# Performance work log

Measured on AMD Instinct MI355X. Metric: run time of the kernel, lower is better.

The kernel has to match this reference:

```python
import jax, jax.numpy as jnp
import numpy as np

B = 2
D = 256
NH = 8
DH = D // NH
L = 4
K = 2                       # sampling grid per box side
NP = K * K                  # sampled points per level
FF = 1024
NQ = 300
NE = 6
ND = 6
REF_SIZE = 4.0
SHAPES = ((64, 64), (32, 32), (16, 16), (8, 8))
S = sum(h * w for h, w in SHAPES)


def make_ref_windows():
    ws = []
    for (H, W) in SHAPES:
        y = (jnp.arange(1, H + 1, dtype=jnp.float32) - 0.5) / (H + 1e-6)
        x = (jnp.arange(1, W + 1, dtype=jnp.float32) - 0.5) / (W + 1e-6)
        yy, xx = jnp.meshgrid(y, x, indexing='ij')
        ctr = jnp.stack([xx, yy], -1).reshape(-1, 2)
        size = jnp.broadcast_to(jnp.array([REF_SIZE / W, REF_SIZE / H], jnp.float32), ctr.shape)
        ws.append(jnp.concatenate([ctr, size], -1))
    return jnp.broadcast_to(jnp.concatenate(ws, 0)[None], (B, S, 4))


def layernorm(x, g, b):
    m = jnp.mean(x, -1, keepdims=True)
    v = jnp.mean((x - m) ** 2, -1, keepdims=True)
    return (x - m) / jnp.sqrt(v + 1e-5) * g + b


def inverse_sigmoid(x, eps=1e-5):
    x = jnp.clip(x, eps, 1.0 - eps)
    return jnp.log(x / (1.0 - x))


def bilinear_sample(vl, pts, Hl, Wl):
    # vl: [B, Hl*Wl, NH, DH], pts: [B, N, NP, 2] normalized to [0,1]
    x = pts[..., 0] * Wl - 0.5
    y = pts[..., 1] * Hl - 0.5
    x0f = jnp.floor(x); y0f = jnp.floor(y)
    wx = x - x0f; wy = y - y0f
    x0 = x0f.astype(jnp.int32); y0 = y0f.astype(jnp.int32)
    Bn, N, P = x.shape

    def gather(yi, xi):
        valid = ((xi >= 0) & (xi < Wl) & (yi >= 0) & (yi < Hl)).astype(vl.dtype)
        idx = jnp.clip(yi, 0, Hl - 1) * Wl + jnp.clip(xi, 0, Wl - 1)
        g = jnp.take_along_axis(vl, idx.reshape(Bn, N * P, 1, 1), axis=1)
        return g.reshape(Bn, N, P, NH, DH) * valid[..., None, None]

    w00 = ((1 - wx) * (1 - wy))[..., None, None]
    w01 = (wx * (1 - wy))[..., None, None]
    w10 = ((1 - wx) * wy)[..., None, None]
    w11 = (wx * wy)[..., None, None]
    return (gather(y0, x0) * w00 + gather(y0, x0 + 1) * w01
            + gather(y0 + 1, x0) * w10 + gather(y0 + 1, x0 + 1) * w11)


def box_attention(q, memory, ref_windows, Wv, bv, Wa, ba, Wo, bo):
    # q: [B,N,D], memory: [B,S,D], ref_windows: [B,N,4] (cx,cy,w,h)
    Bn, N, _ = q.shape
    v = (memory @ Wv + bv).reshape(Bn, memory.shape[1], NH, DH)
    attn = jax.nn.softmax((q @ Wa + ba).reshape(Bn, N, NH, L * NP), axis=-1)
    g = (jnp.arange(K, dtype=jnp.float32) + 0.5) / K - 0.5   # grid fractions in box
    gy, gx = jnp.meshgrid(g, g, indexing='ij')
    grid = jnp.stack([gx.ravel(), gy.ravel()], -1)           # [NP,2]
    pts = ref_windows[:, :, None, :2] + grid[None, None] * ref_windows[:, :, None, 2:]
    out = jnp.zeros((Bn, N, NH, DH), q.dtype)
    start = 0
    for l, (Hl, Wl) in enumerate(SHAPES):
        sl = Hl * Wl
        sampled = bilinear_sample(v[:, start:start + sl], pts, Hl, Wl)  # [B,N,NP,NH,DH]
        out = out + jnp.einsum('bnphd,bnhp->bnhd', sampled, attn[..., l * NP:(l + 1) * NP])
        start += sl
    return out.reshape(Bn, N, D) @ Wo + bo


def mha(q_in, k_in, v_in, Wqkv, bqkv, Wo, bo):
    Bn, N, _ = q_in.shape
    q = (q_in @ Wqkv[:, :D] + bqkv[:D]).reshape(Bn, N, NH, DH)
    k = (k_in @ Wqkv[:, D:2 * D] + bqkv[D:2 * D]).reshape(Bn, N, NH, DH)
    v = (v_in @ Wqkv[:, 2 * D:] + bqkv[2 * D:]).reshape(Bn, N, NH, DH)
    a = jax.nn.softmax(jnp.einsum('bqhd,bkhd->bhqk', q, k) / jnp.sqrt(jnp.float32(DH)), axis=-1)
    o = jnp.einsum('bhqk,bkhd->bqhd', a, v).reshape(Bn, N, D)
    return o @ Wo + bo


def pos_embed_2d(coords):
    # coords: [B,N,2] -> [B,N,D] sine embedding (deformable-DETR style)
    npf = D // 2
    dim_t = 10000.0 ** (2.0 * (jnp.arange(npf) // 2) / npf)
    p = coords[..., None] * (2 * np.pi) / dim_t               # [B,N,2,npf]
    p = jnp.stack([jnp.sin(p[..., 0::2]), jnp.cos(p[..., 1::2])], -1)
    return p.reshape(coords.shape[0], coords.shape[1], 2 * npf)


def reference(src, pos, eWv, ebv, eWa, eba, eWo, ebo, eW1, eb1, eW2, eb2,
              en1g, en1b, en2g, en2b,
              dWqkv, dbqkv, dWso, dbso, dWv, dbv, dWa, dba, dWo, dbo,
              dW1, db1, dW2, db2, dn1g, dn1b, dn2g, dn2b, dn3g, dn3b,
              cls_w, cls_b, bb_w1, bb_b1, bb_w2, bb_b2, bb_w3, bb_b3,
              el_w, el_b, el_g, el_beta):
    ref_windows = make_ref_windows()
    out = src
    for i in range(NE):
        a = box_attention(out + pos, out, ref_windows, eWv[i], ebv[i], eWa[i], eba[i], eWo[i], ebo[i])
        out = layernorm(out + a, en1g[i], en1b[i])
        f = jax.nn.relu(out @ eW1[i] + eb1[i]) @ eW2[i] + eb2[i]
        out = layernorm(out + f, en2g[i], en2b[i])
    # proposal selection (topk + gather)
    valid = jnp.all((ref_windows[..., :2] > 0.01) & (ref_windows[..., :2] < 0.99), axis=-1)
    logits = (out @ cls_w + cls_b)[..., 0]
    logits = jnp.where(valid, logits, -65504.0)
    _, idx = jax.lax.top_k(logits, NQ)
    q_emb = jnp.take_along_axis(out, idx[..., None], axis=1)
    tgt = layernorm(jax.lax.stop_gradient(q_emb) @ el_w + el_b, el_g, el_beta)
    ref_sel = jnp.take_along_axis(ref_windows, idx[..., None], axis=1)
    h = jax.nn.relu(q_emb @ bb_w1 + bb_b1)
    h = jax.nn.relu(h @ bb_w2 + bb_b2)
    tmp = h @ bb_w3 + bb_b3 + inverse_sigmoid(ref_sel)
    out_ref = jax.lax.stop_gradient(jax.nn.sigmoid(tmp))
    query_pos = pos_embed_2d(out_ref[..., :2]) + pos_embed_2d(out_ref[..., 2:])
    # decoder
    x = tgt
    inter = []
    for i in range(ND):
        qk = x + query_pos
        sa = mha(qk, qk, x, dWqkv[i], dbqkv[i], dWso[i], dbso[i])
        x = layernorm(x + sa, dn1g[i], dn1b[i])
        ca = box_attention(x + query_pos, out, out_ref, dWv[i], dbv[i], dWa[i], dba[i], dWo[i], dbo[i])
        x = layernorm(x + ca, dn2g[i], dn2b[i])
        f = jax.nn.relu(x @ dW1[i] + db1[i]) @ dW2[i] + db2[i]
        x = layernorm(x + f, dn3g[i], dn3b[i])
        inter.append(x)
    return jnp.stack(inter)  # [ND, B, NQ, D]


def setup_inputs() -> dict:
    key = jax.random.key(0)
    kit = iter(jax.random.split(key, 80))
    def rn(shape, s=0.02):
        return jax.random.normal(next(kit), shape, jnp.float32) * s
    z = lambda *sh: jnp.zeros(sh, jnp.float32)
    o = lambda *sh: jnp.ones(sh, jnp.float32)
    A = NH * L * NP
    return dict(
        src=jax.random.normal(next(kit), (B, S, D), jnp.float32),
        pos=jax.random.normal(next(kit), (B, S, D), jnp.float32),
        eWv=rn((NE, D, D)), ebv=z(NE, D), eWa=rn((NE, D, A)), eba=z(NE, A),
        eWo=rn((NE, D, D)), ebo=z(NE, D),
        eW1=rn((NE, D, FF)), eb1=z(NE, FF), eW2=rn((NE, FF, D)), eb2=z(NE, D),
        en1g=o(NE, D), en1b=z(NE, D), en2g=o(NE, D), en2b=z(NE, D),
        dWqkv=rn((ND, D, 3 * D)), dbqkv=z(ND, 3 * D),
        dWso=rn((ND, D, D)), dbso=z(ND, D),
        dWv=rn((ND, D, D)), dbv=z(ND, D), dWa=rn((ND, D, A)), dba=z(ND, A),
        dWo=rn((ND, D, D)), dbo=z(ND, D),
        dW1=rn((ND, D, FF)), db1=z(ND, FF), dW2=rn((ND, FF, D)), db2=z(ND, D),
        dn1g=o(ND, D), dn1b=z(ND, D), dn2g=o(ND, D), dn2b=z(ND, D), dn3g=o(ND, D), dn3b=z(ND, D),
        cls_w=rn((D, 1)), cls_b=z(1),
        bb_w1=rn((D, D)), bb_b1=z(D), bb_w2=rn((D, D)), bb_b2=z(D),
        bb_w3=rn((D, 4)), bb_b3=z(4),
        el_w=rn((D, D)), el_b=z(D), el_g=o(D), el_beta=z(D),
    )
```

## Files before the change

kernel.cpp:

```cpp
#include <hip/hip_runtime.h>
#include <hip/hip_bf16.h>
#include <math.h>

typedef unsigned short u16;
typedef unsigned int u32;
typedef unsigned long long u64;

#define Bc   2
#define NHc  8
#define Sc   5440
#define NQc  300
#define NEc  6
#define NDc  6
#define FFc  1024
#define BSc  (Bc*Sc)
#define BNQc (Bc*NQc)

__device__ __forceinline__ float us2f(u16 u) {
    union { float f; unsigned v; } x; x.v = ((unsigned)u) << 16; return x.f;
}

__device__ __forceinline__ u16 f2bf(float f) {
    unsigned u = __float_as_uint(f);
    unsigned r = u + 0x7FFFu + ((u >> 16) & 1u);
    return (u16)(r >> 16);
}
__device__ __forceinline__ float bf2f(u16 u) { return us2f(u); }
__device__ __forceinline__ unsigned pk2(u16 a, u16 b) { return (unsigned)a | ((unsigned)b << 16); }

__device__ __forceinline__ size_t pidx(int row, int k) {
    return (size_t)(k >> 5) * ((size_t)BSc * 32) + ((size_t)row << 5) + (size_t)(k & 31);
}

__device__ __forceinline__ int xcd_swz(int orig, int nwg) {
    int xcd = orig & 7;
    int q = nwg >> 3, r = nwg & 7;
    int base = (xcd < r) ? xcd * (q + 1) : r * (q + 1) + (xcd - r) * q;
    return base + (orig >> 3);
}

using bf16x8 = __attribute__((ext_vector_type(8))) short;
using f32x4  = __attribute__((ext_vector_type(4))) float;

__global__ void k_detect(const u16* __restrict__ src, int* __restrict__ flag) {
    __shared__ int cnt;
    if (threadIdx.x == 0) cnt = 0;
    __syncthreads();
    u16 v = src[threadIdx.x];
    int e = (v >> 7) & 0xFF;
    int plaus = (e == 0) || (e >= 107 && e <= 131);
    atomicAdd(&cnt, plaus);
    __syncthreads();
    if (threadIdx.x == 0) *flag = (cnt >= 224) ? 1 : 0;
}

struct CvtArgs {
    const void* in[48];
    long off[48];
    int n[48];
    int cnt;
    long total;
    u64 skip;
};
__global__ void k_cvt_all8(CvtArgs args, float* __restrict__ out,
                           const int* __restrict__ flag) {
    long g = ((long)blockIdx.x * 256 + threadIdx.x) * 8;
    if (g >= args.total) return;
    int lo = 0, hi = args.cnt - 1;
    while (lo < hi) {
        int mid = (lo + hi + 1) >> 1;
        if (args.off[mid] <= g) lo = mid; else hi = mid - 1;
    }
    long local = g - args.off[lo];
    long n = (long)args.n[lo];
    float v[8];
#pragma unroll
    for (int j = 0; j < 8; ++j) v[j] = 0.f;
    if (*flag) {
        if ((args.skip >> lo) & 1) return;
        const u16* p = (const u16*)args.in[lo] + local;
        if (local + 8 <= n) {
            uint4 r = *(const uint4*)p;
            const u16* pu = (const u16*)&r;
#pragma unroll
            for (int j = 0; j < 8; ++j) v[j] = us2f(pu[j]);
        } else {
            for (int j = 0; j < 8; ++j)
                if (local + j < n) v[j] = us2f(p[j]);
        }
    } else {
        const float* p = (const float*)args.in[lo] + local;
        if (local + 8 <= n) {
            float4 a = ((const float4*)p)[0];
            float4 b = ((const float4*)p)[1];
            v[0] = a.x; v[1] = a.y; v[2] = a.z; v[3] = a.w;
            v[4] = b.x; v[5] = b.y; v[6] = b.z; v[7] = b.w;
        } else {
            for (int j = 0; j < 8; ++j)
                if (local + j < n) v[j] = p[j];
        }
    }
    float4 o0, o1;
    o0.x = v[0]; o0.y = v[1]; o0.z = v[2]; o0.w = v[3];
    o1.x = v[4]; o1.y = v[5]; o1.z = v[6]; o1.w = v[7];
    ((float4*)(out + g))[0] = o0;
    ((float4*)(out + g))[1] = o1;
}

__global__ void k_addf2(const float* __restrict__ a, const float* __restrict__ pos,
                        u16* __restrict__ ah, u16* __restrict__ al,
                        u16* __restrict__ ph, u16* __restrict__ pl, int n) {
    int i = blockIdx.x * 256 + threadIdx.x;
    if (i >= n) return;
    int row = i >> 8, k = i & 255;
    size_t px = pidx(row, k);
    float x = a[i];
    u16 h = f2bf(x);
    ah[px] = h;
    al[px] = f2bf(x - bf2f(h));
    float s = x + pos[i];
    u16 h2 = f2bf(s);
    ph[px] = h2;
    pl[px] = f2bf(s - bf2f(h2));
}

template<int RELU>
__global__ __launch_bounds__(256) void k_mgemm(
    const u16* __restrict__ Ah, const u16* __restrict__ Al,
    const float* __restrict__ W, const u16* __restrict__ Wraw, int ldw,
    size_t wstride,
    const float* __restrict__ bias, int bstride,
    float* __restrict__ C, size_t cstride,
    u16* __restrict__ Ch, u16* __restrict__ Cl,
    int ldc, int K,
    const int* __restrict__ flag) {
    __shared__ __align__(16) u16 lsAH[4096];
    __shared__ __align__(16) u16 lsAL[4096];
    __shared__ __align__(16) u16 lsBH[4096];
    __shared__ __align__(16) u16 lsBL[4096];
    const int t = threadIdx.x;
    int lin = blockIdx.x + gridDim.x * blockIdx.y;
    lin = xcd_swz(lin, gridDim.x * gridDim.y);
    const int row0 = (lin / gridDim.x) * 128, col0 = (lin % gridDim.x) * 128;
    const int z = blockIdx.z;
    const int fast = *flag;
    const size_t PSLAB = (size_t)BSc * 32;
    W += (size_t)z * wstride;
    Wraw += (size_t)z * wstride;
    C += (size_t)z * cstride;
    bias += (size_t)z * bstride;

    const int c0 = t, c1 = 256 + t;
    const size_t abase = (size_t)row0 * 32;
    const u16* a0h = Ah + abase + (size_t)c0 * 8;
    const u16* a1h = Ah + abase + (size_t)c1 * 8;
    const u16* a0l = Al + abase + (size_t)c0 * 8;
    const u16* a1l = Al + abase + (size_t)c1 * 8;
    const unsigned d0 = (((unsigned)c0 & ~3u) | (((unsigned)c0 & 3u) ^ (((unsigned)c0 >> 3) & 3u))) * 8u;
    const unsigned d1 = (((unsigned)c1 & ~3u) | (((unsigned)c1 & 3u) ^ (((unsigned)c1 >> 3) & 3u))) * 8u;

    const int bkp = t >> 4, bno = t & 15;
    const float* bp = W + (size_t)(bkp * 2) * ldw + col0 + bno * 8;
    const u16*  brp = Wraw + (size_t)(bkp * 2) * ldw + col0 + bno * 8;

    const int lane = t & 63;
    const int w = t >> 6;
    const int wr = (w >> 1) * 64, wc = (w & 1) * 64;
    const int kg = lane >> 4, lr = lane & 15;

    unsigned iaf[4];
#pragma unroll
    for (int mi = 0; mi < 4; ++mi) {
        int arow = wr + mi * 16 + lr;
        iaf[mi] = ((unsigned)(arow << 2) + ((unsigned)kg ^ (((unsigned)arow >> 1) & 3u))) * 8u;
    }

    f32x4 acc[4][4] = {};
    uint4 aU0h, aU1h, aU0l, aU1l;
    float4 bR[4];
    uint4 bU0, bU1;
    aU0h = *(const uint4*)a0h;
    aU1h = *(const uint4*)a1h;
    aU0l = *(const uint4*)a0l;
    aU1l = *(const uint4*)a1l;
    if (fast) {
        bU0 = *(const uint4*)brp;
        bU1 = *(const uint4*)(brp + ldw);
    } else {
        const float4* q0 = (const float4*)bp;
        const float4* q1 = (const float4*)(bp + ldw);
        bR[0] = q0[0]; bR[1] = q0[1]; bR[2] = q1[0]; bR[3] = q1[1];
    }

    for (int k0 = 0; k0 < K; k0 += 32) {
        if (k0) __syncthreads();
        *(uint4*)&lsAH[d0] = aU0h;
        *(uint4*)&lsAH[d1] = aU1h;
        *(uint4*)&lsAL[d0] = aU0l;
        *(uint4*)&lsAL[d1] = aU1l;
        {
            unsigned bb = (unsigned)(bkp >> 2) * 1024u + (unsigned)(bkp & 3) * 2u;
            if (fast) {
                const u16* e0 = (const u16*)&bU0;
                const u16* e1 = (const u16*)&bU1;
#pragma unroll
                for (int j = 0; j < 8; ++j) {
                    int slot = bno * 8 + (j ^ (bno & 7));
                    *(unsigned*)&lsBH[bb + (unsigned)slot * 8u] = pk2(e0[j], e1[j]);
                }
            } else {
                float e0f[8], e1f[8];
                *(float4*)&e0f[0] = bR[0]; *(float4*)&e0f[4] = bR[1];
                *(float4*)&e1f[0] = bR[2]; *(float4*)&e1f[4] = bR[3];
#pragma unroll
                for (int j = 0; j < 8; ++j) {
                    int slot = bno * 8 + (j ^ (bno & 7));
                    u16 h0 = f2bf(e0f[j]), h1 = f2bf(e1f[j]);
                    *(unsigned*)&lsBH[bb + (unsigned)slot * 8u] = pk2(h0, h1);
                    u16 l0 = f2bf(e0f[j] - bf2f(h0));
                    u16 l1 = f2bf(e1f[j] - bf2f(h1));
                    *(unsigned*)&lsBL[bb + (unsigned)slot * 8u] = pk2(l0, l1);
                }
            }
        }
        __syncthreads();
        if (k0 + 32 < K) {
            size_t soff = (size_t)((k0 >> 5) + 1) * PSLAB;
            aU0h = *(const uint4*)(a0h + soff);
            aU1h = *(const uint4*)(a1h + soff);
            aU0l = *(const uint4*)(a0l + soff);
            aU1l = *(const uint4*)(a1l + soff);
            if (fast) {
                bU0 = *(const uint4*)(brp + (size_t)(k0 + 32) * ldw);
                bU1 = *(const uint4*)(brp + (size_t)(k0 + 33) * ldw);
            } else {
                const float4* q0 = (const float4*)(bp + (size_t)(k0 + 32) * ldw);
                const float4* q1 = (const float4*)(bp + (size_t)(k0 + 33) * ldw);
                bR[0] = q0[0]; bR[1] = q0[1]; bR[2] = q1[0]; bR[3] = q1[1];
            }
        }
        bf16x8 aH[4], aL[4], bH[4], bL[4];
#pragma unroll
        for (int mi = 0; mi < 4; ++mi) {
            aH[mi] = *(const bf16x8*)&lsAH[iaf[mi]];
            aL[mi] = *(const bf16x8*)&lsAL[iaf[mi]];
        }
#pragma unroll
        for (int ni = 0; ni < 4; ++ni) {
            int c = wc + ni * 16 + lr;
            int slot = (c & ~7) | ((c ^ (c >> 3)) & 7);
            unsigned ib = (unsigned)kg * 1024u + (unsigned)slot * 8u;
            bH[ni] = *(const bf16x8*)&lsBH[ib];
            if (!fast) bL[ni] = *(const bf16x8*)&lsBL[ib];
        }
#pragma unroll
        for (int mi = 0; mi < 4; ++mi)
#pragma unroll
            for (int ni = 0; ni < 4; ++ni) {
                acc[mi][ni] = __builtin_amdgcn_mfma_f32_16x16x32_bf16(aH[mi], bH[ni], acc[mi][ni], 0, 0, 0);
                acc[mi][ni] = __builtin_amdgcn_mfma_f32_16x16x32_bf16(aL[mi], bH[ni], acc[mi][ni], 0, 0, 0);
            }
        if (!fast) {
#pragma unroll
            for (int mi = 0; mi < 4; ++mi)
#pragma unroll
                for (int ni = 0; ni < 4; ++ni)
                    acc[mi][ni] = __builtin_amdgcn_mfma_f32_16x16x32_bf16(aH[mi], bL[ni], acc[mi][ni], 0, 0, 0);
        }
    }
    const int rb = row0 + wr + (lane >> 4) * 4;
#pragma unroll
    for (int ni = 0; ni < 4; ++ni) {
        int cc = col0 + wc + ni * 16 + lr;
        float bv = bias[cc];
#pragma unroll
        for (int mi = 0; mi < 4; ++mi) {
#pragma unroll
            for (int r2 = 0; r2 < 4; ++r2) {
                int rr = rb + mi * 16 + r2;
                float v = acc[mi][ni][r2] + bv;
                if (RELU) v = fmaxf(v, 0.f);
                if (C) C[(size_t)rr * ldc + cc] = v;
                if (Ch) {
                    size_t px = pidx(rr, cc);
                    u16 h = f2bf(v);
                    Ch[px] = h;
                    Cl[px] = f2bf(v - bf2f(h));
                }
            }
        }
    }
}

template<int RELU>
__global__ __launch_bounds__(256) void k_dgemm(
    const float* __restrict__ A, int lda,
    const float* __restrict__ W, int ldw, int wcol0,
    const float* __restrict__ bias,
    float* __restrict__ C, int ldc,
    int M, int N, int K) {
    __shared__ float As[2][16][68];
    __shared__ float Bs[2][16][68];
    int t = threadIdx.x;
    int row0 = blockIdx.y * 64, col0 = blockIdx.x * 64;
    int ti = t >> 4, tj = t & 15;
    int arow = t >> 2, akq = (t & 3) << 2;
    int bk = t >> 4, bn = (t & 15) << 2;
    bool aok = (row0 + arow) < M;
    const float* ap = A + (size_t)(row0 + arow) * lda + akq;
    const float* bp = W + (size_t)bk * ldw + wcol0 + col0 + bn;
    float4 aR = aok ? *(const float4*)ap : make_float4(0.f, 0.f, 0.f, 0.f);
    float4 bR = *(const float4*)bp;
    As[0][akq + 0][arow] = aR.x;
    As[0][akq + 1][arow] = aR.y;
    As[0][akq + 2][arow] = aR.z;
    As[0][akq + 3][arow] = aR.w;
    *(float4*)&Bs[0][bk][bn] = bR;
    __syncthreads();
    int cur = 0;
    float acc[4][4] = {};
    for (int k0 = 0; k0 < K; k0 += 16) {
        bool more = (k0 + 16) < K;
        if (more) {
            aR = aok ? *(const float4*)(ap + k0 + 16) : make_float4(0.f, 0.f, 0.f, 0.f);
            bR = *(const float4*)(bp + (size_t)(k0 + 16) * ldw);
        }
#pragma unroll
        for (int k = 0; k < 16; ++k) {
            float a[4], b[4];
#pragma unroll
            for (int r = 0; r < 4; ++r) a[r] = As[cur][k][ti * 4 + r];
#pragma unroll
            for (int c = 0; c < 4; ++c) b[c] = Bs[cur][k][tj * 4 + c];
#pragma unroll
            for (int r = 0; r < 4; ++r)
#pragma unroll
                for (int c = 0; c < 4; ++c) acc[r][c] += a[r] * b[c];
        }
        if (more) {
            int nxt = cur ^ 1;
            As[nxt][akq + 0][arow] = aR.x;
            As[nxt][akq + 1][arow] = aR.y;
            As[nxt][akq + 2][arow] = aR.z;
            As[nxt][akq + 3][arow] = aR.w;
            *(float4*)&Bs[nxt][bk][bn] = bR;
            __syncthreads();
            cur = nxt;
        }
    }
    for (int r = 0; r < 4; ++r) {
        int rr = row0 + ti * 4 + r;
        if (rr >= M) continue;
        for (int c = 0; c < 4; ++c) {
            int cc = col0 + tj * 4 + c;
            float v = acc[r][c] + bias[cc];
            if (RELU) v = fmaxf(v, 0.f);
            C[(size_t)rr * ldc + cc] = v;
        }
    }
}

__global__ __launch_bounds__(256) void k_gemm4(
    const float* __restrict__ A, const float* __restrict__ W,
    const float* __restrict__ bias, const float* __restrict__ rsel,
    float* __restrict__ oref, int M, int K) {
    int row = blockIdx.x * 64 + (threadIdx.x >> 2);
    int col = threadIdx.x & 3;
    if (row >= M) return;
    float acc = 0.f;
    const float* a = A + (size_t)row * K;
    for (int k = 0; k < K; ++k) acc += a[k] * W[k * 4 + col];
    float tmp = acc + bias[col];
    float r = rsel[(size_t)row * 4 + col];
    r = fminf(fmaxf(r, 1e-5f), 1.f - 1e-5f);
    float v = tmp + logf(r / (1.f - r));
    oref[(size_t)row * 4 + col] = 1.f / (1.f + __expf(-v));
}

__global__ void k_ln(const float* __restrict__ a, const float* __restrict__ b,
                     const float* __restrict__ g, const float* __restrict__ be,
                     float* __restrict__ o,
                     u16* __restrict__ oh, u16* __restrict__ ol,
                     const float* __restrict__ padd, float* __restrict__ opadd,
                     u16* __restrict__ oph, u16* __restrict__ opl,
                     void* __restrict__ sdst, size_t soff,
                     const int* __restrict__ flag) {
    int row = blockIdx.x;
    int t = threadIdx.x;
    __shared__ float red[256];
    size_t ix = (size_t)row * 256 + t;
    float x = a[ix];
    if (b) x += b[ix];
    red[t] = x;
    __syncthreads();
    for (int s = 128; s > 0; s >>= 1) { if (t < s) red[t] += red[t + s]; __syncthreads(); }
    float mean = red[0] / 256.f;
    __syncthreads();
    float d = x - mean;
    red[t] = d * d;
    __syncthreads();
    for (int s = 128; s > 0; s >>= 1) { if (t < s) red[t] += red[t + s]; __syncthreads(); }
    float var = red[0] / 256.f;
    float y = d * rsqrtf(var + 1e-5f) * g[t] + be[t];
    o[ix] = y;
    if (oh) {
        size_t px = pidx(row, t);
        u16 h = f2bf(y);
        oh[px] = h;
        ol[px] = f2bf(y - bf2f(h));
    }
    if (padd) {
        float z = y + padd[ix];
        if (opadd) opadd[ix] = z;
        if (oph) {
            size_t px = pidx(row, t);
            u16 h = f2bf(z);
            oph[px] = h;
            opl[px] = f2bf(z - bf2f(h));
        }
    }
    if (sdst) {
        if (*flag) ((__hip_bfloat16*)sdst)[soff + ix] = __float2bfloat16(y);
        else       ((float*)sdst)[soff + ix] = y;
    }
}

__global__ void k_refw(float* __restrict__ rw) {
    int s = blockIdx.x * 256 + threadIdx.x;
    if (s >= Sc) return;
    int start, HW;
    if (s < 4096)      { start = 0;    HW = 64; }
    else if (s < 5120) { start = 4096; HW = 32; }
    else if (s < 5376) { start = 5120; HW = 16; }
    else               { start = 5376; HW = 8;  }
    int loc = s - start;
    int i = loc / HW, j = loc % HW;
    rw[s * 4 + 0] = (j + 0.5f) / ((float)HW + 1e-6f);
    rw[s * 4 + 1] = (i + 0.5f) / ((float)HW + 1e-6f);
    rw[s * 4 + 2] = 4.0f / (float)HW;
    rw[s * 4 + 3] = 4.0f / (float)HW;
}

__global__ __launch_bounds__(256) void k_box_sample4(
    const float* __restrict__ v, const float* __restrict__ attn,
    const float* __restrict__ refw, int ref_bs,
    float* __restrict__ out, u16* __restrict__ outh, u16* __restrict__ outl,
    int N) {
    const int t = threadIdx.x;
    const int qi = t >> 6, lane = t & 63;
    const int blk = xcd_swz(blockIdx.x, gridDim.x);
    const int n = blk * 4 + qi;
    const int b = blockIdx.y;
    if (n >= N) return;
    const float* arow = attn + ((size_t)b * N + n) * 128;
    float2 wl = *(const float2*)(arow + lane * 2);
    float m = fmaxf(wl.x, wl.y);
#pragma unroll
    for (int d2 = 1; d2 < 8; d2 <<= 1) m = fmaxf(m, __shfl_xor(m, d2, 8));
    float e0 = __expf(wl.x - m), e1 = __expf(wl.y - m);
    float s = e0 + e1;
#pragma unroll
    for (int d2 = 1; d2 < 8; d2 <<= 1) s += __shfl_xor(s, d2, 8);
    float inv = 1.f / s;
    e0 *= inv; e1 *= inv;

    const float* rw = refw + (size_t)ref_bs * b + (size_t)n * 4;
    float cx = rw[0], cy = rw[1], bw = rw[2], bh = rw[3];
    const float* vb = v + (size_t)b * Sc * 256 + lane * 4;
    float4 acc = make_float4(0.f, 0.f, 0.f, 0.f);
    int start = 0;
    const int HWs[4] = {64, 32, 16, 8};
#pragma unroll
    for (int l = 0; l < 4; ++l) {
        int HW = HWs[l];
#pragma unroll
        for (int p = 0; p < 4; ++p) {
            float gx = (p & 1) ? 0.25f : -0.25f;
            float gy = (p >> 1) ? 0.25f : -0.25f;
            float x = (cx + gx * bw) * (float)HW - 0.5f;
            float y = (cy + gy * bh) * (float)HW - 0.5f;
            float x0f = floorf(x), y0f = floorf(y);
            float wx = x - x0f, wy = y - y0f;
            int x0 = (int)x0f, y0 = (int)y0f;
            float4 smp = make_float4(0.f, 0.f, 0.f, 0.f);
            if (x0 >= 0 && x0 < HW && y0 >= 0 && y0 < HW) {
                float4 g4 = *(const float4*)(vb + (size_t)(start + y0 * HW + x0) * 256);
                float wgt = (1.f - wx) * (1.f - wy);
                smp.x += wgt * g4.x; smp.y += wgt * g4.y; smp.z += wgt * g4.z; smp.w += wgt * g4.w;
            }
            if (x0 + 1 >= 0 && x0 + 1 < HW && y0 >= 0 && y0 < HW) {
                float4 g4 = *(const float4*)(vb + (size_t)(start + y0 * HW + x0 + 1) * 256);
                float wgt = wx * (1.f - wy);
                smp.x += wgt * g4.x; smp.y += wgt * g4.y; smp.z += wgt * g4.z; smp.w += wgt * g4.w;
            }
            if (x0 >= 0 && x0 < HW && y0 + 1 >= 0 && y0 + 1 < HW) {
                float4 g4 = *(const float4*)(vb + (size_t)(start + (y0 + 1) * HW + x0) * 256);
                float wgt = (1.f - wx) * wy;
                smp.x += wgt * g4.x; smp.y += wgt * g4.y; smp.z += wgt * g4.z; smp.w += wgt * g4.w;
            }
            if (x0 + 1 >= 0 && x0 + 1 < HW && y0 + 1 >= 0 && y0 + 1 < HW) {
                float4 g4 = *(const float4*)(vb + (size_t)(start + (y0 + 1) * HW + x0 + 1) * 256);
                float wgt = wx * wy;
                smp.x += wgt * g4.x; smp.y += wgt * g4.y; smp.z += wgt * g4.z; smp.w += wgt * g4.w;
            }
            const int idx = l * 4 + p;
            float wsel = (idx & 1) ? e1 : e0;
            float wv = __shfl(wsel, (lane & ~7) | (idx >> 1), 64);
            acc.x += wv * smp.x; acc.y += wv * smp.y;
            acc.z += wv * smp.z; acc.w += wv * smp.w;
        }
        start += HW * HW;
    }
    if (out) {
        size_t obase = ((size_t)b * N + n) * 256 + lane * 4;
        *(float4*)(out + obase) = acc;
    }
    if (outh) {
        size_t px = pidx(b * N + n, lane * 4);
        ushort4 h, lo;
        h.x = f2bf(acc.x); h.y = f2bf(acc.y); h.z = f2bf(acc.z); h.w = f2bf(acc.w);
        lo.x = f2bf(acc.x - bf2f(h.x)); lo.y = f2bf(acc.y - bf2f(h.y));
        lo.z = f2bf(acc.z - bf2f(h.z)); lo.w = f2bf(acc.w - bf2f(h.w));
        *(ushort4*)(outh + px) = h;
        *(ushort4*)(outl + px) = lo;
    }
}

__global__ void k_cls(const float* __restrict__ x, const float* __restrict__ w,
                      const float* __restrict__ cb, const float* __restrict__ rw,
                      float* __restrict__ logits) {
    int row = blockIdx.x;
    int t = threadIdx.x;
    __shared__ float red[256];
    red[t] = x[(size_t)row * 256 + t] * w[t];
    __syncthreads();
    for (int s = 128; s > 0; s >>= 1) { if (t < s) red[t] += red[t + s]; __syncthreads(); }
    if (t == 0) {
        int s = row % Sc;
        float cx = rw[s * 4], cy = rw[s * 4 + 1];
        bool valid = (cx > 0.01f) && (cx < 0.99f) && (cy > 0.01f) && (cy < 0.99f);
        logits[row] = valid ? (red[0] + cb[0]) : -65504.0f;
    }
}

__global__ void k_topk(const float* __restrict__ logits, int* __restrict__ idxout) {
    int b = blockIdx.x;
    int t = threadIdx.x;
    __shared__ unsigned keys[Sc];
    __shared__ int hist[256];
    __shared__ int suf[257];
    __shared__ unsigned sprefix;
    __shared__ int sR;
    __shared__ int cnt;
    __shared__ u64 cand[512];
    for (int i = t; i < Sc; i += 256) {
        union { float f; unsigned u; } x;
        x.f = logits[(size_t)b * Sc + i];
        unsigned u = x.u;
        keys[i] = (u & 0x80000000u) ? ~u : (u | 0x80000000u);
    }
    if (t == 0) { sprefix = 0; sR = NQc; suf[256] = 0; }
    __syncthreads();
    for (int shift = 24; shift >= 0; shift -= 8) {
        hist[t] = 0;
        __syncthreads();
        unsigned pref = sprefix;
        int R = sR;
        unsigned pmask = (shift == 24) ? 0u : (0xFFFFFFFFu << (shift + 8));
        for (int i = t; i < Sc; i += 256) {
            unsigned kk = keys[i];
            if ((kk & pmask) == (pref & pmask))
                atomicAdd(&hist[(kk >> shift) & 255], 1);
        }
        __syncthreads();
        suf[t] = hist[t];
        __syncthreads();
        for (int s2 = 1; s2 < 256; s2 <<= 1) {
            int vv = suf[t] + ((t + s2 < 256) ? suf[t + s2] : 0);
            __syncthreads();
            suf[t] = vv;
            __syncthreads();
        }
        if (suf[t] >= R && suf[t + 1] < R) {
            sR = R - suf[t + 1];
            sprefix = pref | ((unsigned)t << shift);
        }
        __syncthreads();
    }
    unsigned T = sprefix;
    if (t == 0) cnt = 0;
    __syncthreads();
    for (int i = t; i < Sc; i += 256) {
        unsigned kk = keys[i];
        if (kk >= T) {
            int slot = atomicAdd(&cnt, 1);
            if (slot < 512)
                cand[slot] = ~((((u64)kk) << 32) | (u64)(0xFFFFFFFFu - (unsigned)i));
        }
    }
    __syncthreads();
    int total = cnt < 512 ? cnt : 512;
    for (int i = t; i < 512; i += 256)
        if (i >= total) cand[i] = 0xFFFFFFFFFFFFFFFFull;
    __syncthreads();
    for (int i = t; i < 512; i += 256) {
        if (i >= total) continue;
        u64 mine = cand[i];
        int rank = 0;
        for (int j = 0; j < 512; ++j) rank += (cand[j] < mine) ? 1 : 0;
        if (rank < NQc) {
            u64 c = ~mine;
            idxout[b * NQc + rank] = (int)(0xFFFFFFFFu - (unsigned)(c & 0xFFFFFFFFull));
        }
    }
}

__global__ void k_gather(const float* __restrict__ x, const float* __restrict__ rw,
                         const int* __restrict__ idx, float* __restrict__ qemb,
                         float* __restrict__ refsel) {
    int q = blockIdx.x, b = blockIdx.y;
    int t = threadIdx.x;
    int id = idx[b * NQc + q];
    qemb[((size_t)b * NQc + q) * 256 + t] = x[((size_t)b * Sc + id) * 256 + t];
    if (t < 4) refsel[((size_t)b * NQc + q) * 4 + t] = rw[id * 4 + t];
}

__global__ void k_qpos(const float* __restrict__ outref, float* __restrict__ qpos) {
    int n = blockIdx.x, b = blockIdx.y;
    int t = threadIdx.x;
    const float* orf = outref + ((size_t)b * NQc + n) * 4;
    int c = t >> 7;
    int j = (t & 127) >> 1;
    int si = t & 1;
    float tj = powf(10000.f, (float)j / 64.f);
    float sc = 6.283185307179586f / tj;
    float v1 = orf[c] * sc;
    float v2 = orf[2 + c] * sc;
    float r = si ? (cosf(v1) + cosf(v2)) : (sinf(v1) + sinf(v2));
    qpos[((size_t)b * NQc + n) * 256 + t] = r;
}

#define NSPL 10
#define SPLW 30
__global__ __launch_bounds__(256) void k_mha2(
    const float* __restrict__ qk, const float* __restrict__ v,
    float* __restrict__ opart, float* __restrict__ mlpart) {
    __shared__ float lsK[SPLW][256];
    __shared__ float lsV[SPLW][256];
    const int t = threadIdx.x;
    const int h = t >> 5, ql = t & 31;
    const int b = blockIdx.y, z = blockIdx.z;
    const int n = blockIdx.x * 32 + ql;
    const bool qok = n < NQc;
    const int kstart = z * SPLW;
    for (int f = t; f < SPLW * 64; f += 256) {
        int r = f >> 6, c4 = f & 63;
        int krow = kstart + r;
        float4 kv = *(const float4*)(qk + (size_t)(b * NQc + krow) * 512 + 256 + c4 * 4);
        float4 vv = *(const float4*)(v + (size_t)(b * NQc + krow) * 256 + c4 * 4);
        *(float4*)&lsK[r][c4 * 4] = kv;
        *(float4*)&lsV[r][c4 * 4] = vv;
    }
    __syncthreads();
    float q[32];
    {
        const float* qp = qk + (size_t)(b * NQc + (qok ? n : 0)) * 512 + h * 32;
#pragma unroll
        for (int j4 = 0; j4 < 8; ++j4) {
            float4 f = ((const float4*)qp)[j4];
            q[j4 * 4 + 0] = f.x; q[j4 * 4 + 1] = f.y;
            q[j4 * 4 + 2] = f.z; q[j4 * 4 + 3] = f.w;
        }
    }
    const float scale = 0.17677669529663688f;
    float s[SPLW];
#pragma unroll
    for (int kk = 0; kk < SPLW; ++kk) {
        float acc = 0.f;
        const float* kr = &lsK[kk][h * 32];
#pragma unroll
        for (int j4 = 0; j4 < 8; ++j4) {
            float4 kf = ((const float4*)kr)[j4];
            acc += q[j4*4+0]*kf.x + q[j4*4+1]*kf.y + q[j4*4+2]*kf.z + q[j4*4+3]*kf.w;
        }
        s[kk] = acc * scale;
    }
    float m = s[0];
#pragma unroll
    for (int kk = 1; kk < SPLW; ++kk) m = fmaxf(m, s[kk]);
    float o[32];
#pragma unroll
    for (int j = 0; j < 32; ++j) o[j] = 0.f;
    float l = 0.f;
#pragma unroll
    for (int kk = 0; kk < SPLW; ++kk) {
        float e = __expf(s[kk] - m);
        l += e;
        const float* vr = &lsV[kk][h * 32];
#pragma unroll
        for (int j4 = 0; j4 < 8; ++j4) {
            float4 vf = ((const float4*)vr)[j4];
            o[j4*4+0] += e * vf.x; o[j4*4+1] += e * vf.y;
            o[j4*4+2] += e * vf.z; o[j4*4+3] += e * vf.w;
        }
    }
    if (qok) {
        float* op = opart + ((size_t)z * BNQc + (size_t)b * NQc + n) * 256 + h * 32;
#pragma unroll
        for (int j4 = 0; j4 < 8; ++j4) {
            float4 f;
            f.x = o[j4*4+0]; f.y = o[j4*4+1]; f.z = o[j4*4+2]; f.w = o[j4*4+3];
            ((float4*)op)[j4] = f;
        }
        float* mlp = mlpart + ((size_t)z * BNQc + (size_t)b * NQc + n) * 16 + h * 2;
        mlp[0] = m; mlp[1] = l;
    }
}

__global__ void k_mha_comb(const float* __restrict__ opart, const float* __restrict__ mlpart,
                           float* __restrict__ out) {
    int row = blockIdx.x;
    int t = threadIdx.x;
    int h = t >> 5;
    float mm[NSPL], ll[NSPL];
    float M = -3.0e38f;
#pragma unroll
    for (int z = 0; z < NSPL; ++z) {
        mm[z] = mlpart[((size_t)z * BNQc + row) * 16 + h * 2];
        ll[z] = mlpart[((size_t)z * BNQc + row) * 16 + h * 2 + 1];
        M = fmaxf(M, mm[z]);
    }
    float denom = 0.f, osum = 0.f;
#pragma unroll
    for (int z = 0; z < NSPL; ++z) {
        float a = __expf(mm[z] - M);
        denom += ll[z] * a;
        osum += opart[((size_t)z * BNQc + row) * 256 + t] * a;
    }
    out[(size_t)row * 256 + t] = osum / denom;
}

extern "C" void kernel_launch(void* const* d_in, const int* in_sizes, int n_in,
                              void* d_out, int out_size, void* d_ws, size_t ws_size,
                              hipStream_t stream) {
    char* base = (char*)d_ws;
    size_t off = 0;
    auto allocB = [&](size_t bytes) {
        char* p = base + off;
        off = (off + bytes + 255) & ~(size_t)255;
        return p;
    };
    int* flag = (int*)allocB(16);
    auto allocF = [&](size_t n) { return (float*)allocB(n * 4); };
    auto allocH = [&](size_t n) { return (u16*)allocB(n * 2); };

    k_detect<<<1, 256, 0, stream>>>((const u16*)d_in[0], flag);

    CvtArgs ca;
    long acc = 0;
    int ninp = n_in < 48 ? n_in : 48;
    for (int i = 0; i < 48; ++i) {
        int idx2 = i < ninp ? i : ninp - 1;
        ca.in[i] = d_in[idx2];
        ca.n[i] = (i < ninp) ? in_sizes[i] : 0;
        ca.off[i] = acc;
        acc += ((long)ca.n[i] + 63) & ~63L;
    }
    ca.cnt = 48;
    ca.total = acc;
    ca.skip = (1ull << 2) | (1ull << 4) | (1ull << 6) | (1ull << 8) |
              (1ull << 10) | (1ull << 20);
    float* cvtbase = allocF((size_t)acc);
    k_cvt_all8<<<(int)((acc / 8 + 255) / 256), 256, 0, stream>>>(ca, cvtbase, flag);
    float* F[48];
    for (int i = 0; i < 48; ++i) F[i] = cvtbase + ca.off[i];

    const size_t BSD = (size_t)BSc * 256;
    float* enc    = F[0];
    u16* encH  = allocH(BSD);  u16* encL  = allocH(BSD);
    u16* pbufH = allocH(BSD);  u16* pbufL = allocH(BSD);
    u16* tbufH = allocH(BSD);  u16* tbufL = allocH(BSD);
    u16* ffnhH = allocH((size_t)BSc * FFc);
    u16* ffnhL = allocH((size_t)BSc * FFc);
    float* vbuf   = allocF(BSD);
    float* vbuf6  = allocF((size_t)NDc * BSD);
    float* gout   = allocF(BSD);
    float* attnb  = allocF((size_t)BSc * 128);
    float* refw   = allocF(Sc * 4);
    float* logit  = allocF(BSc);
    int*   idx    = (int*)allocB(BNQc * 4);
    float* qemb   = allocF((size_t)BNQc * 256);
    float* rsel   = allocF(BNQc * 4);
    float* xbuf   = allocF((size_t)BNQc * 256);
    float* qposb  = allocF((size_t)BNQc * 256);
    float* dqk    = allocF((size_t)BNQc * 256);
    float* dqk512 = allocF((size_t)BNQc * 512);
    float* dv     = allocF((size_t)BNQc * 256);
    float* dt1    = allocF((size_t)BNQc * 256);
    float* dt2    = allocF((size_t)BNQc * 256);
    float* datt   = allocF((size_t)BNQc * 128);
    float* dffnh  = allocF((size_t)BNQc * FFc);
    float* h1f    = allocF((size_t)BNQc * 256);
    float* h2f    = allocF((size_t)BNQc * 256);
    float* oref   = allocF(BNQc * 4);
    float* opart  = allocF((size_t)NSPL * BNQc * 256);
    float* mlpart = allocF((size_t)NSPL * BNQc * 16);
    (void)ws_size; (void)out_size;

    auto MG = [&](int relu, const u16* Ah, const u16* Al, int widx, size_t woff, int ldw,
                  const float* bias, float* Cf, u16* Ch, u16* Cl, int ldc, int N, int K,
                  int nz, size_t wstride, int bstride, size_t cstride) {
        const float* Wf = F[widx] + woff;
        const u16* Wraw = (const u16*)d_in[widx] + woff;
        dim3 g(N / 128, BSc / 128, nz);
        if (relu) k_mgemm<1><<<g, 256, 0, stream>>>(Ah, Al, Wf, Wraw, ldw, wstride,
                                                    bias, bstride, Cf, cstride, Ch, Cl, ldc, K, flag);
        else      k_mgemm<0><<<g, 256, 0, stream>>>(Ah, Al, Wf, Wraw, ldw, wstride,
                                                    bias, bstride, Cf, cstride, Ch, Cl, ldc, K, flag);
    };
    auto DG = [&](int relu, const float* A, int lda, const float* W, int ldw, int wcol0,
                  const float* bias, float* C, int ldc, int M, int N, int K) {
        dim3 g(N / 64, (M + 63) / 64);
        if (relu) k_dgemm<1><<<g, 256, 0, stream>>>(A, lda, W, ldw, wcol0, bias, C, ldc, M, N, K);
        else      k_dgemm<0><<<g, 256, 0, stream>>>(A, lda, W, ldw, wcol0, bias, C, ldc, M, N, K);
    };

    const int nBSD = (int)BSD;
    k_refw<<<(Sc + 255) / 256, 256, 0, stream>>>(refw);
    k_addf2<<<(nBSD + 255) / 256, 256, 0, stream>>>(enc, F[1], encH, encL, pbufH, pbufL, nBSD);

    for (int i = 0; i < NEc; ++i) {
        MG(0, encH, encL, 2, (size_t)i * 65536, 256, F[3] + i * 256, vbuf, nullptr, nullptr,
           256, 256, 256, 1, 0, 0, 0);
        MG(0, pbufH, pbufL, 4, (size_t)i * 32768, 128, F[5] + i * 128, attnb, nullptr, nullptr,
           128, 128, 256, 1, 0, 0, 0);
        k_box_sample4<<<dim3((Sc + 3) / 4, Bc), 256, 0, stream>>>(vbuf, attnb, refw, 0,
                                                                  nullptr, tbufH, tbufL, Sc);
        MG(0, tbufH, tbufL, 6, (size_t)i * 65536, 256, F[7] + i * 256, gout, nullptr, nullptr,
           256, 256, 256, 1, 0, 0, 0);
        k_ln<<<BSc, 256, 0, stream>>>(enc, gout, F[12] + i * 256, F[13] + i * 256,
                                      enc, encH, encL,
                                      nullptr, nullptr, nullptr, nullptr,
                                      nullptr, 0, flag);
        MG(1, encH, encL, 8, (size_t)i * 262144, 1024, F[9] + i * 1024,
           nullptr, ffnhH, ffnhL, 1024, 1024, 256, 1, 0, 0, 0);
        MG(0, ffnhH, ffnhL, 10, (size_t)i * 262144, 256, F[11] + i * 256,
           gout, nullptr, nullptr, 256, 256, 1024, 1, 0, 0, 0);
        k_ln<<<BSc, 256, 0, stream>>>(enc, gout, F[14] + i * 256, F[15] + i * 256,
                                      enc, encH, encL,
                                      (i < NEc - 1) ? F[1] : nullptr, nullptr,
                                      (i < NEc - 1) ? pbufH : nullptr,
                                      (i < NEc - 1) ? pbufL : nullptr,
                                      nullptr, 0, flag);
    }

    k_cls<<<BSc, 256, 0, stream>>>(enc, F[36], F[37], refw, logit);
    k_topk<<<Bc, 256, 0, stream>>>(logit, idx);
    k_gather<<<dim3(NQc, Bc), 256, 0, stream>>>(enc, refw, idx, qemb, rsel);
    MG(0, encH, encL, 20, 0, 256, F[21], vbuf6, nullptr, nullptr,
       256, 256, 256, NDc, 65536, 256, BSD);
    DG(0, qemb, 256, F[44], 256, 0, F[45], dt1, 256, BNQc, 256, 256);
    DG(1, qemb, 256, F[38], 256, 0, F[39], h1f, 256, BNQc, 256, 256);
    DG(1, h1f,  256, F[40], 256, 0, F[41], h2f, 256, BNQc, 256, 256);
    k_gemm4<<<(BNQc + 63) / 64, 256, 0, stream>>>(h2f, F[42], F[43], rsel, oref, BNQc, 256);
    k_qpos<<<dim3(NQc, Bc), 256, 0, stream>>>(oref, qposb);
    k_ln<<<BNQc, 256, 0, stream>>>(dt1, nullptr, F[46], F[47],
                                   xbuf, nullptr, nullptr,
                                   qposb, dqk, nullptr, nullptr,
                                   nullptr, 0, flag);

    const int nXD = BNQc * 256;
    for (int i = 0; i < NDc; ++i) {
        DG(0, dqk,  256, F[16] + (size_t)i * 196608, 768, 0,   F[17] + i * 768,       dqk512, 512, BNQc, 512, 256);
        DG(0, xbuf, 256, F[16] + (size_t)i * 196608, 768, 512, F[17] + i * 768 + 512, dv,     256, BNQc, 256, 256);
        k_mha2<<<dim3((NQc + 31) / 32, Bc, NSPL), 256, 0, stream>>>(dqk512, dv, opart, mlpart);
        k_mha_comb<<<BNQc, 256, 0, stream>>>(opart, mlpart, dt1);
        DG(0, dt1, 256, F[18] + (size_t)i * 65536, 256, 0, F[19] + i * 256, dt2, 256, BNQc, 256, 256);
        k_ln<<<BNQc, 256, 0, stream>>>(xbuf, dt2, F[30] + i * 256, F[31] + i * 256,
                                       xbuf, nullptr, nullptr,
                                       qposb, dqk, nullptr, nullptr,
                                       nullptr, 0, flag);
        DG(0, dqk, 256, F[22] + (size_t)i * 32768, 128, 0, F[23] + i * 128, datt, 128, BNQc, 128, 256);
        k_box_sample4<<<dim3((NQc + 3) / 4, Bc), 256, 0, stream>>>(vbuf6 + (size_t)i * BSD, datt,
                                                                   oref, NQc * 4,
                                                                   dt1, nullptr, nullptr, NQc);
        DG(0, dt1, 256, F[24] + (size_t)i * 65536, 256, 0, F[25] + i * 256, dt2, 256, BNQc, 256, 256);
        k_ln<<<BNQc, 256, 0, stream>>>(xbuf, dt2, F[32] + i * 256, F[33] + i * 256,
                                       xbuf, nullptr, nullptr,
                                       nullptr, nullptr, nullptr, nullptr,
                                       nullptr, 0, flag);
        DG(1, xbuf,  256,  F[26] + (size_t)i * 262144, 1024, 0, F[27] + i * 1024, dffnh, 1024, BNQc, 1024, 256);
        DG(0, dffnh, 1024, F[28] + (size_t)i * 262144, 256,  0, F[29] + i * 256,  dt2,   256,  BNQc, 256, 1024);
        k_ln<<<BNQc, 256, 0, stream>>>(xbuf, dt2, F[34] + i * 256, F[35] + i * 256,
                                       xbuf, nullptr, nullptr,
                                       (i < NDc - 1) ? qposb : nullptr,
                                       (i < NDc - 1) ? dqk : nullptr, nullptr, nullptr,
                                       d_out, (size_t)i * nXD, flag);
    }
}
```

Baseline: 2.737 ms.

## Split K across two wave groups in encoder GEMM with LDS reduction

```diff
diff --git a/kernel.cpp b/kernel.cpp
--- a/kernel.cpp
+++ b/kernel.cpp
@@ -125,7 +125,7 @@
 }
 
 template<int RELU>
-__global__ __launch_bounds__(256) void k_mgemm(
+__global__ __launch_bounds__(512) void k_mgemm(
     const u16* __restrict__ Ah, const u16* __restrict__ Al,
     const float* __restrict__ W, const u16* __restrict__ Wraw, int ldw,
     size_t wstride,
@@ -134,10 +134,7 @@
     u16* __restrict__ Ch, u16* __restrict__ Cl,
     int ldc, int K,
     const int* __restrict__ flag) {
-    __shared__ __align__(16) u16 lsAH[4096];
-    __shared__ __align__(16) u16 lsAL[4096];
-    __shared__ __align__(16) u16 lsBH[4096];
-    __shared__ __align__(16) u16 lsBL[4096];
+    __shared__ __align__(16) u16 lds16[32768];
     const int t = threadIdx.x;
     int lin = blockIdx.x + gridDim.x * blockIdx.y;
     lin = xcd_swz(lin, gridDim.x * gridDim.y);
@@ -150,22 +147,32 @@
     C += (size_t)z * cstride;
     bias += (size_t)z * bstride;
 
-    const int c0 = t, c1 = 256 + t;
+    const int w = t >> 6, lane = t & 63;
+    const int kh = w >> 2, wl = w & 3;
+    const int th = t & 255;
+    const int K2 = K >> 1;
+    const int nslab = K2 >> 5;
+    const size_t baseOff = (size_t)(kh * nslab) * PSLAB;
+
+    u16* LAH = lds16 + (kh << 12);
+    u16* LAL = lds16 + 8192 + (kh << 12);
+    u16* LBH = lds16 + 16384 + (kh << 12);
+    u16* LBL = lds16 + 24576 + (kh << 12);
+
+    const int c0 = th, c1 = 256 + th;
     const size_t abase = (size_t)row0 * 32;
-    const u16* a0h = Ah + abase + (size_t)c0 * 8;
-    const u16* a1h = Ah + abase + (size_t)c1 * 8;
-    const u16* a0l = Al + abase + (size_t)c0 * 8;
-    const u16* a1l = Al + abase + (size_t)c1 * 8;
+    const u16* a0h = Ah + abase + (size_t)c0 * 8 + baseOff;
+    const u16* a1h = Ah + abase + (size_t)c1 * 8 + baseOff;
+    const u16* a0l = Al + abase + (size_t)c0 * 8 + baseOff;
+    const u16* a1l = Al + abase + (size_t)c1 * 8 + baseOff;
     const unsigned d0 = (((unsigned)c0 & ~3u) | (((unsigned)c0 & 3u) ^ (((unsigned)c0 >> 3) & 3u))) * 8u;
     const unsigned d1 = (((unsigned)c1 & ~3u) | (((unsigned)c1 & 3u) ^ (((unsigned)c1 >> 3) & 3u))) * 8u;
 
-    const int bkp = t >> 4, bno = t & 15;
-    const float* bp = W + (size_t)(bkp * 2) * ldw + col0 + bno * 8;
-    const u16*  brp = Wraw + (size_t)(bkp * 2) * ldw + col0 + bno * 8;
-
-    const int lane = t & 63;
-    const int w = t >> 6;
-    const int wr = (w >> 1) * 64, wc = (w & 1) * 64;
+    const int bkp = th >> 4, bno = th & 15;
+    const float* bp = W + (size_t)(kh * K2 + bkp * 2) * ldw + col0 + bno * 8;
+    const u16*  brp = Wraw + (size_t)(kh * K2 + bkp * 2) * ldw + col0 + bno * 8;
+
+    const int wr = (wl >> 1) * 64, wc = (wl & 1) * 64;
     const int kg = lane >> 4, lr = lane & 15;
 
     unsigned iaf[4];
@@ -192,12 +199,12 @@
         bR[0] = q0[0]; bR[1] = q0[1]; bR[2] = q1[0]; bR[3] = q1[1];
     }
 
-    for (int k0 = 0; k0 < K; k0 += 32) {
+    for (int k0 = 0; k0 < K2; k0 += 32) {
         if (k0) __syncthreads();
-        *(uint4*)&lsAH[d0] = aU0h;
-        *(uint4*)&lsAH[d1] = aU1h;
-        *(uint4*)&lsAL[d0] = aU0l;
-        *(uint4*)&lsAL[d1] = aU1l;
+        *(uint4*)&LAH[d0] = aU0h;
+        *(uint4*)&LAH[d1] = aU1h;
+        *(uint4*)&LAL[d0] = aU0l;
+        *(uint4*)&LAL[d1] = aU1l;
         {
             unsigned bb = (unsigned)(bkp >> 2) * 1024u + (unsigned)(bkp & 3) * 2u;
             if (fast) {
@@ -206,7 +213,7 @@
 #pragma unroll
                 for (int j = 0; j < 8; ++j) {
                     int slot = bno * 8 + (j ^ (bno & 7));
-                    *(unsigned*)&lsBH[bb + (unsigned)slot * 8u] = pk2(e0[j], e1[j]);
+                    *(unsigned*)&LBH[bb + (unsigned)slot * 8u] = pk2(e0[j], e1[j]);
                 }
             } else {
                 float e0f[8], e1f[8];
@@ -216,15 +223,15 @@
                 for (int j = 0; j < 8; ++j) {
                     int slot = bno * 8 + (j ^ (bno & 7));
                     u16 h0 = f2bf(e0f[j]), h1 = f2bf(e1f[j]);
-                    *(unsigned*)&lsBH[bb + (unsigned)slot * 8u] = pk2(h0, h1);
+                    *(unsigned*)&LBH[bb + (unsigned)slot * 8u] = pk2(h0, h1);
                     u16 l0 = f2bf(e0f[j] - bf2f(h0));
                     u16 l1 = f2bf(e1f[j] - bf2f(h1));
-                    *(unsigned*)&lsBL[bb + (unsigned)slot * 8u] = pk2(l0, l1);
+                    *(unsigned*)&LBL[bb + (unsigned)slot * 8u] = pk2(l0, l1);
                 }
             }
         }
         __syncthreads();
-        if (k0 + 32 < K) {
+        if (k0 + 32 < K2) {
             size_t soff = (size_t)((k0 >> 5) + 1) * PSLAB;
             aU0h = *(const uint4*)(a0h + soff);
             aU1h = *(const uint4*)(a1h + soff);
@@ -242,16 +249,16 @@
         bf16x8 aH[4], aL[4], bH[4], bL[4];
 #pragma unroll
         for (int mi = 0; mi < 4; ++mi) {
-            aH[mi] = *(const bf16x8*)&lsAH[iaf[mi]];
-            aL[mi] = *(const bf16x8*)&lsAL[iaf[mi]];
+            aH[mi] = *(const bf16x8*)&LAH[iaf[mi]];
+            aL[mi] = *(const bf16x8*)&LAL[iaf[mi]];
         }
 #pragma unroll
         for (int ni = 0; ni < 4; ++ni) {
             int c = wc + ni * 16 + lr;
             int slot = (c & ~7) | ((c ^ (c >> 3)) & 7);
             unsigned ib = (unsigned)kg * 1024u + (unsigned)slot * 8u;
-            bH[ni] = *(const bf16x8*)&lsBH[ib];
-            if (!fast) bL[ni] = *(const bf16x8*)&lsBL[ib];
+            bH[ni] = *(const bf16x8*)&LBH[ib];
+            if (!fast) bL[ni] = *(const bf16x8*)&LBL[ib];
         }
 #pragma unroll
         for (int mi = 0; mi < 4; ++mi)
@@ -268,24 +275,40 @@
                     acc[mi][ni] = __builtin_amdgcn_mfma_f32_16x16x32_bf16(aH[mi], bL[ni], acc[mi][ni], 0, 0, 0);
         }
     }
-    const int rb = row0 + wr + (lane >> 4) * 4;
-#pragma unroll
-    for (int ni = 0; ni < 4; ++ni) {
-        int cc = col0 + wc + ni * 16 + lr;
-        float bv = bias[cc];
-#pragma unroll
-        for (int mi = 0; mi < 4; ++mi) {
-#pragma unroll
-            for (int r2 = 0; r2 < 4; ++r2) {
-                int rr = rb + mi * 16 + r2;
-                float v = acc[mi][ni][r2] + bv;
-                if (RELU) v = fmaxf(v, 0.f);
-                if (C) C[(size_t)rr * ldc + cc] = v;
-                if (Ch) {
-                    size_t px = pidx(rr, cc);
-                    u16 h = f2bf(v);
-                    Ch[px] = h;
-                    Cl[px] = f2bf(v - bf2f(h));
+    __syncthreads();
+    float* scr = (float*)lds16;
+    if (kh == 1) {
+        float* s = scr + (size_t)th * 64;
+#pragma unroll
+        for (int ni = 0; ni < 4; ++ni)
+#pragma unroll
+            for (int mi = 0; mi < 4; ++mi)
+#pragma unroll
+                for (int r2 = 0; r2 < 4; ++r2)
+                    s[(ni * 4 + mi) * 4 + r2] = acc[mi][ni][r2];
+    }
+    __syncthreads();
+    if (kh == 0) {
+        const float* s = scr + (size_t)th * 64;
+        const int rb = row0 + wr + (lane >> 4) * 4;
+#pragma unroll
+        for (int ni = 0; ni < 4; ++ni) {
+            int cc = col0 + wc + ni * 16 + lr;
+            float bv = bias[cc];
+#pragma unroll
+            for (int mi = 0; mi < 4; ++mi) {
+#pragma unroll
+                for (int r2 = 0; r2 < 4; ++r2) {
+                    int rr = rb + mi * 16 + r2;
+                    float v = acc[mi][ni][r2] + s[(ni * 4 + mi) * 4 + r2] + bv;
+                    if (RELU) v = fmaxf(v, 0.f);
+                    if (C) C[(size_t)rr * ldc + cc] = v;
+                    if (Ch) {
+                        size_t px = pidx(rr, cc);
+                        u16 h = f2bf(v);
+                        Ch[px] = h;
+                        Cl[px] = f2bf(v - bf2f(h));
+                    }
                 }
             }
         }
@@ -813,9 +836,9 @@
         const float* Wf = F[widx] + woff;
         const u16* Wraw = (const u16*)d_in[widx] + woff;
         dim3 g(N / 128, BSc / 128, nz);
-        if (relu) k_mgemm<1><<<g, 256, 0, stream>>>(Ah, Al, Wf, Wraw, ldw, wstride,
+        if (relu) k_mgemm<1><<<g, 512, 0, stream>>>(Ah, Al, Wf, Wraw, ldw, wstride,
                                                     bias, bstride, Cf, cstride, Ch, Cl, ldc, K, flag);
-        else      k_mgemm<0><<<g, 256, 0, stream>>>(Ah, Al, Wf, Wraw, ldw, wstride,
+        else      k_mgemm<0><<<g, 512, 0, stream>>>(Ah, Al, Wf, Wraw, ldw, wstride,
                                                     bias, bstride, Cf, cstride, Ch, Cl, ldc, K, flag);
     };
     auto DG = [&](int relu, const float* A, int lda, const float* W, int ldw, int wcol0,
```

Measured after the change: 2.928 ms. +7.0%, slower.
